# Optimization experiments

Measured on AMD Instinct MI355X. Metric: run time of the kernel, lower is better.

Reference implementation:

```python
import jax, jax.numpy as jnp
import numpy as np

C = 256
D = C // 8  # 32


def setup_inputs() -> dict:
    key = jax.random.key(0)
    ks = jax.random.split(key, 9)
    B, H, W = 4, 64, 64
    x = jax.random.normal(ks[0], (B, C, H, W), dtype=jnp.float32)
    # 1x1 conv weights stored as [out, in] matrices (kernel_size=1)
    s = 1.0 / np.sqrt(C)
    Wf = jax.random.uniform(ks[1], (D, C), jnp.float32, -s, s)
    Wg = jax.random.uniform(ks[2], (D, C), jnp.float32, -s, s)
    Wh = jax.random.uniform(ks[3], (D, C), jnp.float32, -s, s)
    sv = 1.0 / np.sqrt(D)
    Wv = jax.random.uniform(ks[4], (C, D), jnp.float32, -sv, sv)
    bf = jnp.zeros((D,), jnp.float32)
    bg = jnp.zeros((D,), jnp.float32)
    bh = jnp.zeros((D,), jnp.float32)
    bv = jax.random.uniform(ks[5], (C,), jnp.float32, -sv, sv)
    # gamma initialized to zero in the module; use a nonzero value so output is non-trivial
    gamma = jnp.array([0.5], jnp.float32)
    return {"x": x, "Wf": Wf, "bf": bf, "Wg": Wg, "bg": bg,
            "Wh": Wh, "bh": bh, "Wv": Wv, "bv": bv, "gamma": gamma}


def reference(x, Wf, bf, Wg, bg, Wh, bh, Wv, bv, gamma):
    B, Cc, Hh, Ww = x.shape
    N = Hh * Ww
    xf = x.reshape(B, Cc, N)  # flatten spatial tokens, [B, C, N]
    # 1x1 convs == channel matmuls
    f = jnp.einsum('dc,bcn->bdn', Wf, xf) + bf[None, :, None]  # [B, D, N]
    g = jnp.einsum('dc,bcn->bdn', Wg, xf) + bg[None, :, None]
    h = jnp.einsum('dc,bcn->bdn', Wh, xf) + bh[None, :, None]
    # unscaled attention: f^T g -> [B, N, N], softmax over last axis
    attn = jax.nn.softmax(jnp.einsum('bdn,bdm->bnm', f, g), axis=-1)
    # h @ attn: out[:, d, m] = sum_n h[:, d, n] * attn[:, n, m]
    sa = jnp.einsum('bdn,bnm->bdm', h, attn)  # [B, D, N]
    # output 1x1 conv D -> C
    o = jnp.einsum('cd,bdn->bcn', Wv, sa) + bv[None, :, None]
    out = gamma[0] * o.reshape(B, Cc, Hh, Ww)
    return out
```

## Files before the change

### kernel.cpp

```cpp
#include <hip/hip_runtime.h>

typedef __bf16 bf16;
typedef bf16 bf16x4 __attribute__((ext_vector_type(4)));
typedef bf16 bf16x8 __attribute__((ext_vector_type(8)));
typedef float f32x4 __attribute__((ext_vector_type(4)));

#define NB 4
#define NC 256
#define ND 32
#define NN 4096
#define MSPLIT 8

__global__ __launch_bounds__(256, 4) void k_fgh(
    const float* __restrict__ x,
    const float* __restrict__ Wf, const float* __restrict__ bfp,
    const float* __restrict__ Wg, const float* __restrict__ bgp,
    const float* __restrict__ Wh, const float* __restrict__ bhp,
    bf16* __restrict__ fT, bf16* __restrict__ gT, bf16* __restrict__ hM)
{
    __shared__ __align__(16) char xb[32 * 512];
    const int b    = blockIdx.y;
    const int rest = blockIdx.x;
    const int n0   = (rest >> 1) * 32;
    const int half = rest & 1;
    const int t    = threadIdx.x;
    const int lane = t & 63;
    const int w    = t >> 6;
    const int l15  = lane & 15;
    const int l4   = lane >> 4;

    {
        const int nl  = t & 31;
        const int swz = (nl & 7) << 4;
        const int chi = (t >> 5) * 8;
        #pragma unroll
        for (int pass = 0; pass < 4; ++pass) {
            int c0 = pass * 64 + chi;
            const float* xp = x + ((size_t)b * NC + c0) * NN + n0 + nl;
            bf16x8 v;
            #pragma unroll
            for (int j = 0; j < 8; ++j) v[j] = (bf16)xp[(size_t)j * NN];
            *reinterpret_cast<bf16x8*>(&xb[nl * 512 + ((c0 * 2) ^ swz)]) = v;
        }
    }
    __syncthreads();

    #pragma unroll
    for (int rep = 0; rep < 2; ++rep) {
        int tk = w + 4 * rep;
        if (tk < 6) {
            const int strip  = tk & 1;
            const int rt     = half * 3 + (tk >> 1);
            const int tensor = rt >> 1;
            const float* Wsel = tensor == 0 ? Wf : tensor == 1 ? Wg : Wh;
            const float* bsel = tensor == 0 ? bfp : tensor == 1 ? bgp : bhp;
            const int drow = (rt & 1) * 16 + l15;
            const int ncol = strip * 16 + l15;
            const int nswz = (ncol & 7) << 4;
            f32x4 acc = {0.f, 0.f, 0.f, 0.f};
            #pragma unroll
            for (int kc = 0; kc < 8; ++kc) {
                const float* wp = Wsel + drow * NC + kc * 32 + l4 * 8;
                f32x4 wlo = *reinterpret_cast<const f32x4*>(wp);
                f32x4 whi = *reinterpret_cast<const f32x4*>(wp + 4);
                bf16x8 a;
                #pragma unroll
                for (int j = 0; j < 4; ++j) {
                    a[j]     = (bf16)wlo[j];
                    a[4 + j] = (bf16)whi[j];
                }
                bf16x8 bb = *reinterpret_cast<const bf16x8*>(
                    &xb[ncol * 512 + ((kc * 64 + l4 * 16) ^ nswz)]);
                acc = __builtin_amdgcn_mfma_f32_16x16x32_bf16(a, bb, acc, 0, 0, 0);
            }
            const int dbase = (rt & 1) * 16 + l4 * 4;
            const int n = n0 + ncol;
            if (tensor < 2) {
                bf16x4 vv;
                #pragma unroll
                for (int r = 0; r < 4; ++r) vv[r] = (bf16)(acc[r] + bsel[dbase + r]);
                bf16* dst = (tensor == 0 ? fT : gT) + ((size_t)b * NN + n) * ND + dbase;
                *reinterpret_cast<bf16x4*>(dst) = vv;
            } else {
                #pragma unroll
                for (int r = 0; r < 4; ++r)
                    hM[((size_t)b * ND + dbase + r) * NN + n] =
                        (bf16)(acc[r] + bsel[dbase + r]);
            }
        }
    }
}

__global__ __launch_bounds__(256) void k_rowsum(
    const bf16* __restrict__ fT, const bf16* __restrict__ gT,
    float* __restrict__ Lpart)
{
    const int b  = blockIdx.z;
    const int ms = blockIdx.y;
    const int nb = blockIdx.x * 64;
    const int t  = threadIdx.x;
    const int lane = t & 63;
    const int w  = t >> 6;
    const int l15 = lane & 15;
    const int l4  = lane >> 4;

    bf16x8 a = *reinterpret_cast<const bf16x8*>(
        fT + ((size_t)b * NN + nb + w * 16 + l15) * ND + l4 * 8);
    float sum0 = 0.f, sum1 = 0.f, sum2 = 0.f, sum3 = 0.f;
    const bf16* gp = gT + (size_t)b * NN * ND
                   + ((size_t)ms * (NN / MSPLIT) + l15) * ND + l4 * 8;
    #pragma unroll 4
    for (int m = 0; m < NN / MSPLIT; m += 32) {
        bf16x8 b0 = *reinterpret_cast<const bf16x8*>(gp + (size_t)m * ND);
        bf16x8 b1 = *reinterpret_cast<const bf16x8*>(gp + (size_t)(m + 16) * ND);
        f32x4 z = {0.f, 0.f, 0.f, 0.f};
        f32x4 s0 = __builtin_amdgcn_mfma_f32_16x16x32_bf16(a, b0, z, 0, 0, 0);
        f32x4 s1 = __builtin_amdgcn_mfma_f32_16x16x32_bf16(a, b1, z, 0, 0, 0);
        sum0 += __expf(s0[0]) + __expf(s1[0]);
        sum1 += __expf(s0[1]) + __expf(s1[1]);
        sum2 += __expf(s0[2]) + __expf(s1[2]);
        sum3 += __expf(s0[3]) + __expf(s1[3]);
    }
    float sv[4] = {sum0, sum1, sum2, sum3};
    #pragma unroll
    for (int r = 0; r < 4; ++r) {
        float v = sv[r];
        v += __shfl_xor(v, 1);
        v += __shfl_xor(v, 2);
        v += __shfl_xor(v, 4);
        v += __shfl_xor(v, 8);
        sv[r] = v;
    }
    if (l15 == 0) {
        #pragma unroll
        for (int r = 0; r < 4; ++r)
            Lpart[((size_t)ms * NB + b) * NN + nb + w * 16 + l4 * 4 + r] = sv[r];
    }
}

__global__ __launch_bounds__(256, 4) void k_attnproj(
    const bf16* __restrict__ fT, const bf16* __restrict__ gT,
    const bf16* __restrict__ hM, const float* __restrict__ Lpart,
    const float* __restrict__ Wv, const float* __restrict__ bv,
    const float* __restrict__ gamma, float* __restrict__ out)
{
    __shared__ __align__(16) char Pl[4 * 2048];
    __shared__ float rlw[4][64];
    __shared__ float sa_s[4][32 * 16];

    const int b  = blockIdx.y;
    const int m0 = blockIdx.x * 16;
    const int t  = threadIdx.x;
    const int lane = t & 63;
    const int w  = t >> 6;
    const int l15 = lane & 15;
    const int l4  = lane >> 4;

    bf16x8 gfrag = *reinterpret_cast<const bf16x8*>(
        gT + ((size_t)b * NN + m0 + l15) * ND + l4 * 8);

    f32x4 acc0 = {0.f, 0.f, 0.f, 0.f};
    f32x4 acc1 = {0.f, 0.f, 0.f, 0.f};

    char* Pw = &Pl[w * 2048];
    const int mswz = (l15 & 7) << 4;
    const bf16* fsrc = fT + (size_t)b * NN * ND;
    const bf16* hsrc = hM + (size_t)b * ND * NN;

    for (int it = 0; it < 16; ++it) {
        const int n1 = it * 256 + w * 64;

        float s = 0.f;
        #pragma unroll
        for (int ms = 0; ms < MSPLIT; ++ms)
            s += Lpart[((size_t)ms * NB + b) * NN + n1 + lane];
        rlw[w][lane] = 1.0f / s;

        #pragma unroll
        for (int nt = 0; nt < 4; ++nt) {
            bf16x8 afrag = *reinterpret_cast<const bf16x8*>(
                fsrc + (size_t)(n1 + nt * 16 + l15) * ND + l4 * 8);
            f32x4 z = {0.f, 0.f, 0.f, 0.f};
            f32x4 sv = __builtin_amdgcn_mfma_f32_16x16x32_bf16(afrag, gfrag, z, 0, 0, 0);
            bf16x4 p4;
            #pragma unroll
            for (int r = 0; r < 4; ++r)
                p4[r] = (bf16)(__expf(sv[r]) * rlw[w][nt * 16 + l4 * 4 + r]);
            *reinterpret_cast<bf16x4*>(
                &Pw[l15 * 128 + ((nt * 32 + l4 * 8) ^ mswz)]) = p4;
        }
        #pragma unroll
        for (int kc = 0; kc < 2; ++kc) {
            bf16x8 pb = *reinterpret_cast<const bf16x8*>(
                &Pw[l15 * 128 + ((kc * 64 + l4 * 16) ^ mswz)]);
            bf16x8 h0 = *reinterpret_cast<const bf16x8*>(
                hsrc + (size_t)l15 * NN + n1 + kc * 32 + l4 * 8);
            acc0 = __builtin_amdgcn_mfma_f32_16x16x32_bf16(h0, pb, acc0, 0, 0, 0);
            bf16x8 h1 = *reinterpret_cast<const bf16x8*>(
                hsrc + (size_t)(16 + l15) * NN + n1 + kc * 32 + l4 * 8);
            acc1 = __builtin_amdgcn_mfma_f32_16x16x32_bf16(h1, pb, acc1, 0, 0, 0);
        }
    }

    #pragma unroll
    for (int r = 0; r < 4; ++r) {
        sa_s[w][(l4 * 4 + r) * 16 + l15]        = acc0[r];
        sa_s[w][(16 + l4 * 4 + r) * 16 + l15]   = acc1[r];
    }
    __syncthreads();

    const int m  = t & 15;
    const int cb = (t >> 4) * 16;
    float sav[32];
    #pragma unroll
    for (int d = 0; d < 32; ++d)
        sav[d] = sa_s[0][d * 16 + m] + sa_s[1][d * 16 + m]
               + sa_s[2][d * 16 + m] + sa_s[3][d * 16 + m];
    const float g0 = gamma[0];
    float* op = out + (size_t)b * NC * NN + m0 + m;
    #pragma unroll
    for (int i = 0; i < 16; ++i) {
        int c = cb + i;
        const float* wp = Wv + c * ND;
        float sum = bv[c];
        #pragma unroll
        for (int d = 0; d < 32; ++d) sum = fmaf(wp[d], sav[d], sum);
        op[(size_t)c * NN] = g0 * sum;
    }
}

extern "C" void kernel_launch(void* const* d_in, const int* in_sizes, int n_in,
                              void* d_out, int out_size, void* d_ws, size_t ws_size,
                              hipStream_t stream)
{
    const float* x   = (const float*)d_in[0];
    const float* Wf  = (const float*)d_in[1];
    const float* bfp = (const float*)d_in[2];
    const float* Wg  = (const float*)d_in[3];
    const float* bgp = (const float*)d_in[4];
    const float* Wh  = (const float*)d_in[5];
    const float* bhp = (const float*)d_in[6];
    const float* Wv  = (const float*)d_in[7];
    const float* bv  = (const float*)d_in[8];
    const float* gm  = (const float*)d_in[9];
    float* outp = (float*)d_out;

    char* ws = (char*)d_ws;
    bf16*  fT    = (bf16*)ws;
    bf16*  gT    = (bf16*)(ws + (1u << 20));
    bf16*  hM    = (bf16*)(ws + (2u << 20));
    float* Lpart = (float*)(ws + (3u << 20));

    k_fgh     <<<dim3(256, NB),        dim3(256), 0, stream>>>(
        x, Wf, bfp, Wg, bgp, Wh, bhp, fT, gT, hM);
    k_rowsum  <<<dim3(64, MSPLIT, NB), dim3(256), 0, stream>>>(fT, gT, Lpart);
    k_attnproj<<<dim3(256, NB),        dim3(256), 0, stream>>>(
        fT, gT, hM, Lpart, Wv, bv, gm, outp);
}
```

Measured before the change: 179.3 us.

## Split attention over key chunks with LDS-staged f/h tiles and separate projection kernel

The fused attention+projection kernel is restructured. Each block now handles 64 query columns (one per wave, 16 each) over one of 8 key-dimension splits. The f and h tiles are shared through double-buffered LDS with register prefetch, replacing per-wave redundant global loads. Partial sa results go to a workspace, and a new projection kernel reduces the splits and applies Wv/bv/gamma with channel splitting. This trades an extra kernel launch and workspace round-trip for less redundant global traffic and more parallelism.

Result: faster. 162.9 us (-9.2%).

```diff
diff --git a/kernel.cpp b/kernel.cpp
--- a/kernel.cpp
+++ b/kernel.cpp
@@ -9,7 +9,9 @@
 #define NC 256
 #define ND 32
 #define NN 4096
+#define NSPLIT 8
 #define MSPLIT 8
+#define CSPL 8
 
 __global__ __launch_bounds__(256, 4) void k_fgh(
     const float* __restrict__ x,
@@ -138,18 +140,19 @@
     }
 }
 
-__global__ __launch_bounds__(256, 4) void k_attnproj(
+__global__ __launch_bounds__(256) void k_attn(
     const bf16* __restrict__ fT, const bf16* __restrict__ gT,
     const bf16* __restrict__ hM, const float* __restrict__ Lpart,
-    const float* __restrict__ Wv, const float* __restrict__ bv,
-    const float* __restrict__ gamma, float* __restrict__ out)
-{
+    float* __restrict__ saWS)
+{
+    __shared__ __align__(16) char fL[2][64 * 80];
+    __shared__ __align__(16) char hL[2][32 * 144];
     __shared__ __align__(16) char Pl[4 * 2048];
-    __shared__ float rlw[4][64];
-    __shared__ float sa_s[4][32 * 16];
-
-    const int b  = blockIdx.y;
-    const int m0 = blockIdx.x * 16;
+    __shared__ float rlL[2][64];
+
+    const int b  = blockIdx.z;
+    const int ns = blockIdx.y;
+    const int m0 = blockIdx.x * 64;
     const int t  = threadIdx.x;
     const int lane = t & 63;
     const int w  = t >> 6;
@@ -157,35 +160,69 @@
     const int l4  = lane >> 4;
 
     bf16x8 gfrag = *reinterpret_cast<const bf16x8*>(
-        gT + ((size_t)b * NN + m0 + l15) * ND + l4 * 8);
+        gT + ((size_t)b * NN + m0 + w * 16 + l15) * ND + l4 * 8);
 
     f32x4 acc0 = {0.f, 0.f, 0.f, 0.f};
     f32x4 acc1 = {0.f, 0.f, 0.f, 0.f};
 
     char* Pw = &Pl[w * 2048];
     const int mswz = (l15 & 7) << 4;
+
+    const int s_nl = t >> 2;
+    const int s_dl = (t & 3) * 8;
+    const int s_d  = t >> 3;
+    const int s_ne = (t & 7) * 8;
     const bf16* fsrc = fT + (size_t)b * NN * ND;
     const bf16* hsrc = hM + (size_t)b * ND * NN;
 
-    for (int it = 0; it < 16; ++it) {
-        const int n1 = it * 256 + w * 64;
-
-        float s = 0.f;
+    const int nbeg = ns * (NN / NSPLIT);
+
+    bf16x8 fv = *reinterpret_cast<const bf16x8*>(
+        fsrc + (size_t)(nbeg + s_nl) * ND + s_dl);
+    bf16x8 hv = *reinterpret_cast<const bf16x8*>(
+        hsrc + (size_t)s_d * NN + nbeg + s_ne);
+    float lsum = 0.f;
+    if (t < 64) {
         #pragma unroll
         for (int ms = 0; ms < MSPLIT; ++ms)
-            s += Lpart[((size_t)ms * NB + b) * NN + n1 + lane];
-        rlw[w][lane] = 1.0f / s;
+            lsum += Lpart[((size_t)ms * NB + b) * NN + nbeg + t];
+    }
+
+    #pragma unroll 2
+    for (int it = 0; it < NN / NSPLIT / 64; ++it) {
+        const int cur = it & 1;
+        const int n1  = nbeg + it * 64;
+
+        *reinterpret_cast<bf16x8*>(&fL[cur][s_nl * 80 + s_dl * 2]) = fv;
+        *reinterpret_cast<bf16x8*>(&hL[cur][s_d * 144 + s_ne * 2]) = hv;
+        if (t < 64) rlL[cur][t] = 1.0f / lsum;
+        __syncthreads();
+
+        if (it + 1 < NN / NSPLIT / 64) {
+            const int n2 = n1 + 64;
+            fv = *reinterpret_cast<const bf16x8*>(
+                fsrc + (size_t)(n2 + s_nl) * ND + s_dl);
+            hv = *reinterpret_cast<const bf16x8*>(
+                hsrc + (size_t)s_d * NN + n2 + s_ne);
+            if (t < 64) {
+                float s = 0.f;
+                #pragma unroll
+                for (int ms = 0; ms < MSPLIT; ++ms)
+                    s += Lpart[((size_t)ms * NB + b) * NN + n2 + t];
+                lsum = s;
+            }
+        }
 
         #pragma unroll
         for (int nt = 0; nt < 4; ++nt) {
             bf16x8 afrag = *reinterpret_cast<const bf16x8*>(
-                fsrc + (size_t)(n1 + nt * 16 + l15) * ND + l4 * 8);
+                &fL[cur][(nt * 16 + l15) * 80 + l4 * 16]);
             f32x4 z = {0.f, 0.f, 0.f, 0.f};
-            f32x4 sv = __builtin_amdgcn_mfma_f32_16x16x32_bf16(afrag, gfrag, z, 0, 0, 0);
+            f32x4 s = __builtin_amdgcn_mfma_f32_16x16x32_bf16(afrag, gfrag, z, 0, 0, 0);
             bf16x4 p4;
             #pragma unroll
             for (int r = 0; r < 4; ++r)
-                p4[r] = (bf16)(__expf(sv[r]) * rlw[w][nt * 16 + l4 * 4 + r]);
+                p4[r] = (bf16)(__expf(s[r]) * rlL[cur][nt * 16 + l4 * 4 + r]);
             *reinterpret_cast<bf16x4*>(
                 &Pw[l15 * 128 + ((nt * 32 + l4 * 8) ^ mswz)]) = p4;
         }
@@ -194,33 +231,55 @@
             bf16x8 pb = *reinterpret_cast<const bf16x8*>(
                 &Pw[l15 * 128 + ((kc * 64 + l4 * 16) ^ mswz)]);
             bf16x8 h0 = *reinterpret_cast<const bf16x8*>(
-                hsrc + (size_t)l15 * NN + n1 + kc * 32 + l4 * 8);
+                &hL[cur][l15 * 144 + kc * 64 + l4 * 16]);
             acc0 = __builtin_amdgcn_mfma_f32_16x16x32_bf16(h0, pb, acc0, 0, 0, 0);
             bf16x8 h1 = *reinterpret_cast<const bf16x8*>(
-                hsrc + (size_t)(16 + l15) * NN + n1 + kc * 32 + l4 * 8);
+                &hL[cur][(16 + l15) * 144 + kc * 64 + l4 * 16]);
             acc1 = __builtin_amdgcn_mfma_f32_16x16x32_bf16(h1, pb, acc1, 0, 0, 0);
         }
     }
 
-    #pragma unroll
-    for (int r = 0; r < 4; ++r) {
-        sa_s[w][(l4 * 4 + r) * 16 + l15]        = acc0[r];
-        sa_s[w][(16 + l4 * 4 + r) * 16 + l15]   = acc1[r];
+    float* sp = saWS + (((size_t)ns * NB + b) * NN + m0 + w * 16 + l15) * ND;
+    *reinterpret_cast<f32x4*>(sp + l4 * 4)      = acc0;
+    *reinterpret_cast<f32x4*>(sp + 16 + l4 * 4) = acc1;
+}
+
+__global__ __launch_bounds__(256) void k_proj(
+    const float* __restrict__ saWS,
+    const float* __restrict__ Wv, const float* __restrict__ bv,
+    const float* __restrict__ gamma, float* __restrict__ out)
+{
+    __shared__ float sa_s[64 * 33];
+    const int b  = blockIdx.z;
+    const int c0 = blockIdx.y * (NC / CSPL);
+    const int m0 = blockIdx.x * 64;
+    const int t  = threadIdx.x;
+
+    #pragma unroll
+    for (int p = t; p < 64 * 8; p += 256) {
+        int m = p >> 3, dq = (p & 7) * 4;
+        float s0 = 0.f, s1 = 0.f, s2 = 0.f, s3 = 0.f;
+        #pragma unroll
+        for (int s4 = 0; s4 < NSPLIT; ++s4) {
+            f32x4 v = *reinterpret_cast<const f32x4*>(
+                saWS + (((size_t)s4 * NB + b) * NN + m0 + m) * ND + dq);
+            s0 += v[0]; s1 += v[1]; s2 += v[2]; s3 += v[3];
+        }
+        float* dp = &sa_s[m * 33 + dq];
+        dp[0] = s0; dp[1] = s1; dp[2] = s2; dp[3] = s3;
     }
     __syncthreads();
 
-    const int m  = t & 15;
-    const int cb = (t >> 4) * 16;
+    const int mloc = t & 63;
+    const int cg   = t >> 6;
     float sav[32];
     #pragma unroll
-    for (int d = 0; d < 32; ++d)
-        sav[d] = sa_s[0][d * 16 + m] + sa_s[1][d * 16 + m]
-               + sa_s[2][d * 16 + m] + sa_s[3][d * 16 + m];
+    for (int d = 0; d < 32; ++d) sav[d] = sa_s[mloc * 33 + d];
     const float g0 = gamma[0];
-    float* op = out + (size_t)b * NC * NN + m0 + m;
-    #pragma unroll
-    for (int i = 0; i < 16; ++i) {
-        int c = cb + i;
+    float* op = out + (size_t)b * NC * NN + m0 + mloc;
+    #pragma unroll
+    for (int i = 0; i < 8; ++i) {
+        int c = c0 + cg * 8 + i;
         const float* wp = Wv + c * ND;
         float sum = bv[c];
         #pragma unroll
@@ -250,10 +309,11 @@
     bf16*  gT    = (bf16*)(ws + (1u << 20));
     bf16*  hM    = (bf16*)(ws + (2u << 20));
     float* Lpart = (float*)(ws + (3u << 20));
-
-    k_fgh     <<<dim3(256, NB),        dim3(256), 0, stream>>>(
+    float* saWS  = (float*)(ws + (3u << 20) + (512u << 10));
+
+    k_fgh   <<<dim3(256, NB),        dim3(256), 0, stream>>>(
         x, Wf, bfp, Wg, bgp, Wh, bhp, fT, gT, hM);
-    k_rowsum  <<<dim3(64, MSPLIT, NB), dim3(256), 0, stream>>>(fT, gT, Lpart);
-    k_attnproj<<<dim3(256, NB),        dim3(256), 0, stream>>>(
-        fT, gT, hM, Lpart, Wv, bv, gm, outp);
-}
+    k_rowsum<<<dim3(64, MSPLIT, NB), dim3(256), 0, stream>>>(fT, gT, Lpart);
+    k_attn  <<<dim3(64, NSPLIT, NB), dim3(256), 0, stream>>>(fT, gT, hM, Lpart, saWS);
+    k_proj  <<<dim3(64, CSPL, NB),   dim3(256), 0, stream>>>(saWS, Wv, bv, gm, outp);
+}
```
